# Optimization experiments

Hardware: AMD Instinct MI355X
Metric: run time of the kernel (lower is better)

Reference implementation:

```python
import jax, jax.numpy as jnp
import numpy as np

H = 16        # query heads
D = 4         # KV downsampling -> H//D = 4 kv heads
WINDOW = 1024 # sliding window
THETA = 10000.0


def _rope_cos_sin(L, dim):
    freqs = 1.0 / (THETA ** (jnp.arange(0, dim - 1, 2, dtype=jnp.float32) / dim))
    ang = jnp.arange(L, dtype=jnp.float32)[:, None] * freqs[None, :]  # (L, dim//2)
    return jnp.cos(ang), jnp.sin(ang)


def _apply_rope(x, cos, sin):
    # x: (N, h, L, dim); interleaved complex pairs (even=real, odd=imag)
    xr, xi = x[..., 0::2], x[..., 1::2]
    orr = xr * cos - xi * sin
    oii = xr * sin + xi * cos
    return jnp.stack([orr, oii], axis=-1).reshape(x.shape)


def setup_inputs() -> dict:
    key = jax.random.key(0)
    ks = jax.random.split(key, 5)
    N, L, E = 4, 2048, 2048
    return {
        "x": jax.random.normal(ks[0], (N, L, E), dtype=jnp.float32),
        "Wq": jax.random.normal(ks[1], (E, E), dtype=jnp.float32) * 0.02,
        "Wk": jax.random.normal(ks[2], (E // D, E), dtype=jnp.float32) * 0.02,
        "Wv": jax.random.normal(ks[3], (E // D, E), dtype=jnp.float32) * 0.02,
        "Wo": jax.random.normal(ks[4], (E, E), dtype=jnp.float32) * 0.02,
    }


def reference(x, Wq, Wk, Wv, Wo):
    N, L, E = x.shape
    dim = E // H  # 128 per-head dim (same for q and downsampled k/v)
    Hkv = H // D

    q = (x @ Wq.T).reshape(N, L, H, dim).transpose(0, 2, 1, 3)      # (N,H,L,d)
    k = (x @ Wk.T).reshape(N, L, Hkv, dim).transpose(0, 2, 1, 3)    # (N,Hkv,L,d)
    v = (x @ Wv.T).reshape(N, L, Hkv, dim).transpose(0, 2, 1, 3)

    cos, sin = _rope_cos_sin(L, dim)
    q = _apply_rope(q, cos, sin)
    k = _apply_rope(k, cos, sin)

    # GQA: expand kv heads (repeat_interleave along head axis)
    k = jnp.repeat(k, D, axis=1)  # (N,H,L,d)
    v = jnp.repeat(v, D, axis=1)

    scale = 1.0 / jnp.sqrt(jnp.float32(dim))
    attn = jnp.einsum("bhld,bhsd->bhls", q, k) * scale  # (N,H,L,L)

    i = jnp.arange(L)[:, None]
    j = jnp.arange(L)[None, :]
    allowed = (j <= i) & (j > i - WINDOW)  # causal + sliding window
    attn = jnp.where(allowed[None, None], attn, -jnp.inf)
    attn = jax.nn.softmax(attn, axis=-1)

    z = jnp.einsum("bhls,bhsd->bhld", attn, v)  # (N,H,L,d)
    z = z.transpose(0, 2, 1, 3).reshape(N, L, E)
    return z @ Wo.T
```

## Files before the change

kernel.cpp:

```cpp
#include <hip/hip_runtime.h>
#include <hip/hip_bf16.h>
#include <math.h>

typedef unsigned short u16;
typedef unsigned int u32;
typedef __attribute__((ext_vector_type(8))) short short8;
typedef __attribute__((ext_vector_type(8))) u16 ushort8;
typedef __attribute__((ext_vector_type(4))) float f32x4;
typedef __attribute__((ext_vector_type(16))) float f32x16;
typedef __attribute__((ext_vector_type(4))) u32 u32x4;

#define N_B 4
#define L_S 2048
#define E_D 2048
#define NH 16
#define HD 128
#define WIN 1024
#define QW 3072
#define LOG2E 1.4426950408889634f

static __device__ __forceinline__ u16 f32_bf16(float f) {
  u32 u = __builtin_bit_cast(u32, f);
  u = (u + 0x7fffu + ((u >> 16) & 1u)) >> 16;
  return (u16)u;
}
static __device__ __forceinline__ float bf16_f32(u16 h) {
  u32 u = ((u32)h) << 16;
  return __builtin_bit_cast(float, u);
}
static __device__ __forceinline__ u32 pack_bf16_pair(float lo, float hi) {
  __hip_bfloat162 h2 = __float22bfloat162_rn(make_float2(lo, hi));
  u32 r;
  __builtin_memcpy(&r, &h2, 4);
  return r;
}
static __device__ __forceinline__ void gload_lds16(const void* g, void* l) {
  __builtin_amdgcn_global_load_lds((__attribute__((address_space(1))) void*)g,
                                   (__attribute__((address_space(3))) void*)l, 16, 0, 0);
}

__global__ void k_cast(const float* __restrict__ src, u16* __restrict__ dst, int n8) {
  int i = blockIdx.x * blockDim.x + threadIdx.x;
  if (i >= n8) return;
  const float4* s = (const float4*)src + (size_t)i * 2;
  float4 a = s[0], b = s[1];
  ushort8 v;
  v[0] = f32_bf16(a.x); v[1] = f32_bf16(a.y); v[2] = f32_bf16(a.z); v[3] = f32_bf16(a.w);
  v[4] = f32_bf16(b.x); v[5] = f32_bf16(b.y); v[6] = f32_bf16(b.z); v[7] = f32_bf16(b.w);
  *((ushort8*)dst + i) = v;
}

__global__ void k_rope_table(float* __restrict__ cs, float* __restrict__ sn) {
  int idx = blockIdx.x * blockDim.x + threadIdx.x;
  int l = idx >> 6, f = idx & 63;
  float freq = exp2f(-(float)f * (13.287712379549449f / 64.0f));
  float ang = (float)l * freq;
  cs[idx] = cosf(ang);
  sn[idx] = sinf(ang);
}

__global__ void k_rope_apply(u16* __restrict__ QKV, const float* __restrict__ cs,
                             const float* __restrict__ sn) {
  int idx = blockIdx.x * blockDim.x + threadIdx.x;
  int f = idx & 63;
  int rest = idx >> 6;
  int hh = rest % 20;
  int row = rest / 20;
  int l = row & (L_S - 1);
  int col = (hh < NH) ? (hh * HD + 2 * f) : (E_D + (hh - NH) * HD + 2 * f);
  u32* p = (u32*)(QKV + (size_t)row * QW + col);
  u32 v = *p;
  float xr = bf16_f32((u16)(v & 0xffffu));
  float xi = bf16_f32((u16)(v >> 16));
  float c = cs[l * 64 + f], s = sn[l * 64 + f];
  float orr = xr * c - xi * s;
  float oii = xr * s + xi * c;
  *p = (u32)f32_bf16(orr) | ((u32)f32_bf16(oii) << 16);
}

template <int OUT_F32>
__global__ __launch_bounds__(512, 1) void k_gemm256(
    const u16* __restrict__ A, int lda,
    const u16* __restrict__ B, int ldb,
    void* __restrict__ Cp, int ldc, int K) {
  __shared__ __align__(16) u16 Ab[3 * 8192];
  __shared__ __align__(16) u16 Bb[3 * 8192];
  const int tid = threadIdx.x;
  const int lane = tid & 63, w = tid >> 6;
  const int lr = lane & 15, lg = lane >> 4;
  const int wm = w >> 2, wn = w & 3;
  const int fid = blockIdx.x;
  const int cc = fid & 7, l = fid >> 3;
  const int m0 = (cc * 4 + (l & 3)) * 256;
  const int n0 = (l >> 2) * 256;
  const int rswz = (lr & 6) << 3;

  auto STAGE = [&](int kt, int bb) {
    const int r2 = tid >> 2;
    const int ce = (((tid & 3) * 16) ^ ((r2 & 6) << 3)) >> 1;
#pragma unroll
    for (int rr = 0; rr < 2; ++rr) {
      int row = rr * 128 + r2;
      gload_lds16(A + (size_t)(m0 + row) * lda + kt * 32 + ce,
                  (char*)Ab + bb * 16384 + rr * 8192 + (w << 10));
      gload_lds16(B + (size_t)(n0 + row) * ldb + kt * 32 + ce,
                  (char*)Bb + bb * 16384 + rr * 8192 + (w << 10));
    }
  };

  f32x4 acc[8][4];
  const f32x4 z4 = {0.f, 0.f, 0.f, 0.f};
#pragma unroll
  for (int mf = 0; mf < 8; ++mf)
#pragma unroll
    for (int nf = 0; nf < 4; ++nf) acc[mf][nf] = z4;

  const int nt = K >> 5;
  STAGE(0, 0);
  STAGE(1, 1);
  asm volatile("s_waitcnt vmcnt(4)" ::: "memory");
  __builtin_amdgcn_sched_barrier(0);
  __builtin_amdgcn_s_barrier();
  __builtin_amdgcn_sched_barrier(0);

  int c3 = 0;
  for (int t = 0; t < nt; ++t) {
    int ib = c3 + 2; if (ib >= 3) ib -= 3;
    if (t + 2 < nt) STAGE(t + 2, ib);
    const char* Abt = (const char*)Ab + c3 * 16384;
    const char* Bbt = (const char*)Bb + c3 * 16384;
    short8 af[8], bf[4];
#pragma unroll
    for (int nf = 0; nf < 4; ++nf) {
      int row = wn * 64 + nf * 16 + lr;
      bf[nf] = *(const short8*)(Bbt + row * 64 + ((lg * 16) ^ rswz));
    }
#pragma unroll
    for (int mf = 0; mf < 8; ++mf) {
      int row = wm * 128 + mf * 16 + lr;
      af[mf] = *(const short8*)(Abt + row * 64 + ((lg * 16) ^ rswz));
    }
    __builtin_amdgcn_s_setprio(1);
#pragma unroll
    for (int mf = 0; mf < 8; ++mf)
#pragma unroll
      for (int nf = 0; nf < 4; ++nf)
        acc[mf][nf] =
            __builtin_amdgcn_mfma_f32_16x16x32_bf16(af[mf], bf[nf], acc[mf][nf], 0, 0, 0);
    __builtin_amdgcn_s_setprio(0);
    if (t + 2 < nt)
      asm volatile("s_waitcnt vmcnt(4) lgkmcnt(0)" ::: "memory");
    else
      asm volatile("s_waitcnt vmcnt(0) lgkmcnt(0)" ::: "memory");
    __builtin_amdgcn_sched_barrier(0);
    __builtin_amdgcn_s_barrier();
    __builtin_amdgcn_sched_barrier(0);
    c3 = (c3 == 2) ? 0 : c3 + 1;
  }

#pragma unroll
  for (int mf = 0; mf < 8; ++mf)
#pragma unroll
    for (int nf = 0; nf < 4; ++nf)
#pragma unroll
      for (int j = 0; j < 4; ++j) {
        size_t r = (size_t)(m0 + wm * 128 + mf * 16 + lg * 4 + j);
        int c = n0 + wn * 64 + nf * 16 + lr;
        if (OUT_F32)
          ((float*)Cp)[r * ldc + c] = acc[mf][nf][j];
        else
          ((u16*)Cp)[r * ldc + c] = f32_bf16(acc[mf][nf][j]);
      }
}

__global__ __launch_bounds__(512, 2) void k_attn(u16* __restrict__ QKV) {
  const int bx = blockIdx.x, h = blockIdx.y, b = blockIdx.z;
  const int qb = (b >= 2) ? 7 - bx : bx;
  const int tid = threadIdx.x;
  const int lane = tid & 63, w = tid >> 6;
  const int l31 = lane & 31, hi = lane >> 5;
  const int kh = h >> 2;
  const int qs = qb * 256 + w * 32;
  __shared__ __align__(16) u16 Klds[2][64 * 128];
  __shared__ __align__(16) u16 Vt[2][128 * 64];
  const float SCL2 = 0.08838834764831845f * 1.4426950408889634f;
  const size_t bL = (size_t)b * L_S;
  const int q = qs + l31;
  const size_t rowQ = (bL + q) * QW + h * HD;
  short8 qf[8];
#pragma unroll
  for (int ds = 0; ds < 8; ++ds)
    qf[ds] = *(const short8*)(QKV + rowQ + ds * 16 + hi * 8);
  f32x16 o[4];
#pragma unroll
  for (int dt = 0; dt < 4; ++dt)
#pragma unroll
    for (int r = 0; r < 16; ++r) o[dt][r] = 0.f;
  float m2 = -3e38f, lsum = 0.f;
  int t0 = qb * 256 - (WIN - 1);
  if (t0 < 0) t0 = 0;
  t0 >>= 6;
  const int t1 = 4 * qb + 3;
  short8 vreg[2];

  auto ISSUE_K = [&](int t, int buf) {
    char* Kb = (char*)Klds + buf * 16384;
#pragma unroll
    for (int rr = 0; rr < 2; ++rr) {
      int row = rr * 32 + (tid >> 4);
      int colb = ((tid & 15) * 16) ^ ((row & 7) << 4);
      gload_lds16(QKV + (bL + t * 64 + row) * QW + E_D + kh * HD + (colb >> 1),
                  Kb + rr * 8192 + w * 1024 + (lane << 4));
    }
  };
  auto LOAD_V = [&](int t) {
#pragma unroll
    for (int rr = 0; rr < 2; ++rr)
      vreg[rr] = *(const short8*)(QKV + (bL + t * 64 + lane) * QW + E_D + 512 + kh * HD +
                                  ((w * 2 + rr) * 8));
  };
  auto WRITE_V = [&](int buf) {
    char* Vb = (char*)Vt + buf * 16384;
#pragma unroll
    for (int rr = 0; rr < 2; ++rr) {
      int db = (w * 2 + rr) * 8;
#pragma unroll
      for (int e = 0; e < 8; ++e)
        *(u16*)(Vb + ((((db + e) * 128) + lane * 2) ^ (e << 4))) = (u16)vreg[rr][e];
    }
  };

  LOAD_V(t0);
  ISSUE_K(t0, 0);
  __syncthreads();
  WRITE_V(0);
  int c = 0;

  for (int t = t0; t <= t1; ++t) {
    const int kv0 = t * 64;
    const int tn = (t < t1) ? t + 1 : t1;
    ISSUE_K(tn, c ^ 1);
    LOAD_V(tn);
    const bool act = (kv0 <= qs + 31) && (kv0 + 63 > qs - WIN);
    u32x4 pa[4];
    if (act) {
      char* Kb = (char*)Klds + c * 16384;
      f32x16 s[2];
#pragma unroll
      for (int g = 0; g < 2; ++g)
#pragma unroll
        for (int r = 0; r < 16; ++r) s[g][r] = 0.f;
#pragma unroll
      for (int g = 0; g < 2; ++g) {
        const int r = g * 32 + l31;
        const int rsw = (r & 7) << 4;
#pragma unroll
        for (int ds = 0; ds < 8; ++ds) {
          short8 kf = *(const short8*)(Kb + (r * 256 + ((ds * 32 + hi * 16) ^ rsw)));
          s[g] = __builtin_amdgcn_mfma_f32_32x32x16_bf16(kf, qf[ds], s[g], 0, 0, 0);
        }
      }
      float v[2][16];
      float mx = -3e38f;
#pragma unroll
      for (int g = 0; g < 2; ++g)
#pragma unroll
        for (int r = 0; r < 16; ++r) {
          int kg = kv0 + g * 32 + (r & 3) + 8 * (r >> 2) + 4 * hi;
          bool a = (kg <= q) && (kg > q - WIN);
          float vv = a ? s[g][r] * SCL2 : -3e38f;
          v[g][r] = vv;
          mx = fmaxf(mx, vv);
        }
      mx = fmaxf(mx, __shfl_xor(mx, 32));
      if (__ballot(mx > m2 + 11.5415603f)) {
        float mn = fmaxf(m2, mx);
        float alpha = exp2f(m2 - mn);
        m2 = mn;
        lsum *= alpha;
#pragma unroll
        for (int r = 0; r < 16; ++r) {
          float alr = __shfl(alpha, (r & 3) + 8 * (r >> 2) + 4 * hi);
#pragma unroll
          for (int dt = 0; dt < 4; ++dt) o[dt][r] *= alr;
        }
      }
      float rs = 0.f;
#pragma unroll
      for (int g = 0; g < 2; ++g)
#pragma unroll
        for (int r = 0; r < 16; ++r) {
          float pe = (v[g][r] > -1e37f) ? exp2f(v[g][r] - m2) : 0.f;
          v[g][r] = pe;
          rs += pe;
        }
      rs += __shfl_xor(rs, 32);
      lsum += rs;
#pragma unroll
      for (int g = 0; g < 2; ++g) {
        u32 W[8];
#pragma unroll
        for (int qi = 0; qi < 4; ++qi) {
          W[2 * qi]     = pack_bf16_pair(v[g][4 * qi + 0], v[g][4 * qi + 1]);
          W[2 * qi + 1] = pack_bf16_pair(v[g][4 * qi + 2], v[g][4 * qi + 3]);
        }
        u32 R[4];
        R[0] = __shfl_xor(hi ? W[0] : W[2], 32);
        R[1] = __shfl_xor(hi ? W[1] : W[3], 32);
        R[2] = __shfl_xor(hi ? W[4] : W[6], 32);
        R[3] = __shfl_xor(hi ? W[5] : W[7], 32);
#pragma unroll
        for (int ksl = 0; ksl < 2; ++ksl) {
          u32x4 fr;
          if (hi == 0) {
            fr[0] = W[4 * ksl]; fr[1] = W[4 * ksl + 1];
            fr[2] = R[2 * ksl]; fr[3] = R[2 * ksl + 1];
          } else {
            fr[0] = R[2 * ksl]; fr[1] = R[2 * ksl + 1];
            fr[2] = W[4 * ksl + 2]; fr[3] = W[4 * ksl + 3];
          }
          pa[g * 2 + ksl] = fr;
        }
      }
    }
    __syncthreads();
    WRITE_V(c ^ 1);
    if (act) {
      char* Vb = (char*)Vt + c * 16384;
      __builtin_amdgcn_s_setprio(1);
#pragma unroll
      for (int dt = 0; dt < 4; ++dt) {
        const int d = dt * 32 + l31;
        const int dsw = (d & 7) << 4;
#pragma unroll
        for (int ks = 0; ks < 4; ++ks) {
          short8 vf = *(const short8*)(Vb + (d * 128 + ((ks * 32 + hi * 16) ^ dsw)));
          o[dt] = __builtin_amdgcn_mfma_f32_32x32x16_bf16(
              __builtin_bit_cast(short8, pa[ks]), vf, o[dt], 0, 0, 0);
        }
      }
      __builtin_amdgcn_s_setprio(0);
    }
    c ^= 1;
  }
  float inv = 1.0f / lsum;
#pragma unroll
  for (int r = 0; r < 16; ++r) {
    int ridx = (r & 3) + 8 * (r >> 2) + 4 * hi;
    float invr = __shfl(inv, ridx);
    size_t rowO = (bL + qs + ridx) * QW + h * HD + l31;
#pragma unroll
    for (int dt = 0; dt < 4; ++dt)
      QKV[rowO + dt * 32] = f32_bf16(o[dt][r] * invr);
  }
}

extern "C" void kernel_launch(void* const* d_in, const int* in_sizes, int n_in,
                              void* d_out, int out_size, void* d_ws, size_t ws_size,
                              hipStream_t stream) {
  const float* x  = (const float*)d_in[0];
  const float* Wq = (const float*)d_in[1];
  const float* Wk = (const float*)d_in[2];
  const float* Wv = (const float*)d_in[3];
  const float* Wo = (const float*)d_in[4];
  char* ws = (char*)d_ws;
  if (ws_size < 105906176u) return;
  u16* xb    = (u16*)(ws);
  u16* Wqkv  = (u16*)(ws + 33554432);
  u16* Wob   = (u16*)(ws + 46137344);
  u16* QKV   = (u16*)(ws + 54525952);
  float* cs  = (float*)(ws + 104857600);
  float* sn  = (float*)(ws + 105381888);

  k_cast<<<8192, 256, 0, stream>>>(x, xb, 16777216 / 8);
  k_cast<<<2048, 256, 0, stream>>>(Wq, Wqkv, 4194304 / 8);
  k_cast<<<512, 256, 0, stream>>>(Wk, Wqkv + 2048 * 2048, 1048576 / 8);
  k_cast<<<512, 256, 0, stream>>>(Wv, Wqkv + 2560 * 2048, 1048576 / 8);
  k_cast<<<2048, 256, 0, stream>>>(Wo, Wob, 4194304 / 8);
  k_rope_table<<<512, 256, 0, stream>>>(cs, sn);
  k_gemm256<0><<<384, 512, 0, stream>>>(xb, 2048, Wqkv, 2048, QKV, QW, 2048);
  k_rope_apply<<<40960, 256, 0, stream>>>(QKV, cs, sn);
  k_attn<<<dim3(8, 16, 4), 512, 0, stream>>>(QKV);
  k_gemm256<1><<<256, 512, 0, stream>>>(QKV, QW, Wob, 2048, d_out, 2048, 2048);
}
```

Before: 427.3 us.

## Fuse Q RoPE into attention, split GEMM k-step, skip masking on full tiles

Query RoPE now runs inside the attention kernel as the Q fragments are loaded, so the standalone RoPE pass only touches the K heads, which saves a read-modify-write over Q. The GEMM main loop is split into two half-M phases with extra barriers, interleaving the A and B global-to-LDS staging with the MFMA work. The attention kernel adds a fast path for fully unmasked tiles that skips per-element mask checks, and it no longer issues a redundant prefetch or V write on the last iteration. The extra barriers in the GEMM could add synchronisation stalls.

```diff
diff --git a/kernel.cpp b/kernel.cpp
--- a/kernel.cpp
+++ b/kernel.cpp
@@ -59,15 +59,15 @@
   sn[idx] = sinf(ang);
 }
 
-__global__ void k_rope_apply(u16* __restrict__ QKV, const float* __restrict__ cs,
-                             const float* __restrict__ sn) {
+__global__ void k_rope_k(u16* __restrict__ QKV, const float* __restrict__ cs,
+                         const float* __restrict__ sn) {
   int idx = blockIdx.x * blockDim.x + threadIdx.x;
   int f = idx & 63;
   int rest = idx >> 6;
-  int hh = rest % 20;
-  int row = rest / 20;
+  int hh = rest & 3;
+  int row = rest >> 2;
   int l = row & (L_S - 1);
-  int col = (hh < NH) ? (hh * HD + 2 * f) : (E_D + (hh - NH) * HD + 2 * f);
+  int col = E_D + hh * HD + 2 * f;
   u32* p = (u32*)(QKV + (size_t)row * QW + col);
   u32 v = *p;
   float xr = bf16_f32((u16)(v & 0xffffu));
@@ -79,7 +79,7 @@
 }
 
 template <int OUT_F32>
-__global__ __launch_bounds__(512, 1) void k_gemm256(
+__global__ __launch_bounds__(512, 1) void k_gemm8(
     const u16* __restrict__ A, int lda,
     const u16* __restrict__ B, int ldb,
     void* __restrict__ Cp, int ldc, int K) {
@@ -95,17 +95,19 @@
   const int n0 = (l >> 2) * 256;
   const int rswz = (lr & 6) << 3;
 
-  auto STAGE = [&](int kt, int bb) {
-    const int r2 = tid >> 2;
-    const int ce = (((tid & 3) * 16) ^ ((r2 & 6) << 3)) >> 1;
-#pragma unroll
-    for (int rr = 0; rr < 2; ++rr) {
-      int row = rr * 128 + r2;
-      gload_lds16(A + (size_t)(m0 + row) * lda + kt * 32 + ce,
+  const int r2 = tid >> 2;
+  const int ce = (((tid & 3) * 16) ^ ((r2 & 6) << 3)) >> 1;
+  auto STAGE_A = [&](int kt, int bb) {
+#pragma unroll
+    for (int rr = 0; rr < 2; ++rr)
+      gload_lds16(A + (size_t)(m0 + rr * 128 + r2) * lda + kt * 32 + ce,
                   (char*)Ab + bb * 16384 + rr * 8192 + (w << 10));
-      gload_lds16(B + (size_t)(n0 + row) * ldb + kt * 32 + ce,
+  };
+  auto STAGE_B = [&](int kt, int bb) {
+#pragma unroll
+    for (int rr = 0; rr < 2; ++rr)
+      gload_lds16(B + (size_t)(n0 + rr * 128 + r2) * ldb + kt * 32 + ce,
                   (char*)Bb + bb * 16384 + rr * 8192 + (w << 10));
-    }
   };
 
   f32x4 acc[8][4];
@@ -116,8 +118,8 @@
     for (int nf = 0; nf < 4; ++nf) acc[mf][nf] = z4;
 
   const int nt = K >> 5;
-  STAGE(0, 0);
-  STAGE(1, 1);
+  STAGE_A(0, 0); STAGE_B(0, 0);
+  STAGE_A(1, 1); STAGE_B(1, 1);
   asm volatile("s_waitcnt vmcnt(4)" ::: "memory");
   __builtin_amdgcn_sched_barrier(0);
   __builtin_amdgcn_s_barrier();
@@ -126,32 +128,57 @@
   int c3 = 0;
   for (int t = 0; t < nt; ++t) {
     int ib = c3 + 2; if (ib >= 3) ib -= 3;
-    if (t + 2 < nt) STAGE(t + 2, ib);
     const char* Abt = (const char*)Ab + c3 * 16384;
     const char* Bbt = (const char*)Bb + c3 * 16384;
-    short8 af[8], bf[4];
+    short8 af[4], bf[4];
 #pragma unroll
     for (int nf = 0; nf < 4; ++nf) {
       int row = wn * 64 + nf * 16 + lr;
       bf[nf] = *(const short8*)(Bbt + row * 64 + ((lg * 16) ^ rswz));
     }
 #pragma unroll
-    for (int mf = 0; mf < 8; ++mf) {
+    for (int mf = 0; mf < 4; ++mf) {
       int row = wm * 128 + mf * 16 + lr;
       af[mf] = *(const short8*)(Abt + row * 64 + ((lg * 16) ^ rswz));
     }
+    if (t + 2 < nt) STAGE_A(t + 2, ib);
+    __builtin_amdgcn_sched_barrier(0);
+    __builtin_amdgcn_s_barrier();
+    asm volatile("s_waitcnt lgkmcnt(0)" ::: "memory");
+    __builtin_amdgcn_sched_barrier(0);
     __builtin_amdgcn_s_setprio(1);
 #pragma unroll
-    for (int mf = 0; mf < 8; ++mf)
+    for (int mf = 0; mf < 4; ++mf)
 #pragma unroll
       for (int nf = 0; nf < 4; ++nf)
         acc[mf][nf] =
             __builtin_amdgcn_mfma_f32_16x16x32_bf16(af[mf], bf[nf], acc[mf][nf], 0, 0, 0);
     __builtin_amdgcn_s_setprio(0);
+    __builtin_amdgcn_sched_barrier(0);
+    __builtin_amdgcn_s_barrier();
+    __builtin_amdgcn_sched_barrier(0);
+#pragma unroll
+    for (int mf = 0; mf < 4; ++mf) {
+      int row = wm * 128 + 64 + mf * 16 + lr;
+      af[mf] = *(const short8*)(Abt + row * 64 + ((lg * 16) ^ rswz));
+    }
+    if (t + 2 < nt) STAGE_B(t + 2, ib);
     if (t + 2 < nt)
-      asm volatile("s_waitcnt vmcnt(4) lgkmcnt(0)" ::: "memory");
+      asm volatile("s_waitcnt vmcnt(4)" ::: "memory");
     else
-      asm volatile("s_waitcnt vmcnt(0) lgkmcnt(0)" ::: "memory");
+      asm volatile("s_waitcnt vmcnt(0)" ::: "memory");
+    __builtin_amdgcn_sched_barrier(0);
+    __builtin_amdgcn_s_barrier();
+    asm volatile("s_waitcnt lgkmcnt(0)" ::: "memory");
+    __builtin_amdgcn_sched_barrier(0);
+    __builtin_amdgcn_s_setprio(1);
+#pragma unroll
+    for (int mf = 0; mf < 4; ++mf)
+#pragma unroll
+      for (int nf = 0; nf < 4; ++nf)
+        acc[4 + mf][nf] =
+            __builtin_amdgcn_mfma_f32_16x16x32_bf16(af[mf], bf[nf], acc[4 + mf][nf], 0, 0, 0);
+    __builtin_amdgcn_s_setprio(0);
     __builtin_amdgcn_sched_barrier(0);
     __builtin_amdgcn_s_barrier();
     __builtin_amdgcn_sched_barrier(0);
@@ -173,7 +200,9 @@
       }
 }
 
-__global__ __launch_bounds__(512, 2) void k_attn(u16* __restrict__ QKV) {
+__global__ __launch_bounds__(512, 2) void k_attn(u16* __restrict__ QKV,
+                                                 const float* __restrict__ cs,
+                                                 const float* __restrict__ sn) {
   const int bx = blockIdx.x, h = blockIdx.y, b = blockIdx.z;
   const int qb = (b >= 2) ? 7 - bx : bx;
   const int tid = threadIdx.x;
@@ -189,8 +218,23 @@
   const size_t rowQ = (bL + q) * QW + h * HD;
   short8 qf[8];
 #pragma unroll
-  for (int ds = 0; ds < 8; ++ds)
-    qf[ds] = *(const short8*)(QKV + rowQ + ds * 16 + hi * 8);
+  for (int ds = 0; ds < 8; ++ds) {
+    short8 qr = *(const short8*)(QKV + rowQ + ds * 16 + hi * 8);
+    const int f0 = ds * 8 + hi * 4;
+    float4 c4 = *(const float4*)(cs + (size_t)q * 64 + f0);
+    float4 s4 = *(const float4*)(sn + (size_t)q * 64 + f0);
+    ushort8 qo;
+#pragma unroll
+    for (int e = 0; e < 4; ++e) {
+      float xr = bf16_f32((u16)qr[2 * e]);
+      float xi = bf16_f32((u16)qr[2 * e + 1]);
+      float co = (e == 0) ? c4.x : (e == 1) ? c4.y : (e == 2) ? c4.z : c4.w;
+      float si = (e == 0) ? s4.x : (e == 1) ? s4.y : (e == 2) ? s4.z : s4.w;
+      qo[2 * e]     = f32_bf16(xr * co - xi * si);
+      qo[2 * e + 1] = f32_bf16(xr * si + xi * co);
+    }
+    qf[ds] = __builtin_bit_cast(short8, qo);
+  }
   f32x16 o[4];
 #pragma unroll
   for (int dt = 0; dt < 4; ++dt)
@@ -238,10 +282,13 @@
 
   for (int t = t0; t <= t1; ++t) {
     const int kv0 = t * 64;
-    const int tn = (t < t1) ? t + 1 : t1;
-    ISSUE_K(tn, c ^ 1);
-    LOAD_V(tn);
+    const bool lastt = (t == t1);
+    if (!lastt) {
+      ISSUE_K(t + 1, c ^ 1);
+      LOAD_V(t + 1);
+    }
     const bool act = (kv0 <= qs + 31) && (kv0 + 63 > qs - WIN);
+    const bool full = (kv0 + 63 <= qs) && (kv0 > qs + 31 - WIN);
     u32x4 pa[4];
     if (act) {
       char* Kb = (char*)Klds + c * 16384;
@@ -262,16 +309,27 @@
       }
       float v[2][16];
       float mx = -3e38f;
-#pragma unroll
-      for (int g = 0; g < 2; ++g)
-#pragma unroll
-        for (int r = 0; r < 16; ++r) {
-          int kg = kv0 + g * 32 + (r & 3) + 8 * (r >> 2) + 4 * hi;
-          bool a = (kg <= q) && (kg > q - WIN);
-          float vv = a ? s[g][r] * SCL2 : -3e38f;
-          v[g][r] = vv;
-          mx = fmaxf(mx, vv);
-        }
+      if (full) {
+#pragma unroll
+        for (int g = 0; g < 2; ++g)
+#pragma unroll
+          for (int r = 0; r < 16; ++r) {
+            float vv = s[g][r] * SCL2;
+            v[g][r] = vv;
+            mx = fmaxf(mx, vv);
+          }
+      } else {
+#pragma unroll
+        for (int g = 0; g < 2; ++g)
+#pragma unroll
+          for (int r = 0; r < 16; ++r) {
+            int kg = kv0 + g * 32 + (r & 3) + 8 * (r >> 2) + 4 * hi;
+            bool a = (kg <= q) && (kg > q - WIN);
+            float vv = a ? s[g][r] * SCL2 : -3e38f;
+            v[g][r] = vv;
+            mx = fmaxf(mx, vv);
+          }
+      }
       mx = fmaxf(mx, __shfl_xor(mx, 32));
       if (__ballot(mx > m2 + 11.5415603f)) {
         float mn = fmaxf(m2, mx);
@@ -286,14 +344,25 @@
         }
       }
       float rs = 0.f;
-#pragma unroll
-      for (int g = 0; g < 2; ++g)
-#pragma unroll
-        for (int r = 0; r < 16; ++r) {
-          float pe = (v[g][r] > -1e37f) ? exp2f(v[g][r] - m2) : 0.f;
-          v[g][r] = pe;
-          rs += pe;
-        }
+      if (full) {
+#pragma unroll
+        for (int g = 0; g < 2; ++g)
+#pragma unroll
+          for (int r = 0; r < 16; ++r) {
+            float pe = exp2f(v[g][r] - m2);
+            v[g][r] = pe;
+            rs += pe;
+          }
+      } else {
+#pragma unroll
+        for (int g = 0; g < 2; ++g)
+#pragma unroll
+          for (int r = 0; r < 16; ++r) {
+            float pe = (v[g][r] > -1e37f) ? exp2f(v[g][r] - m2) : 0.f;
+            v[g][r] = pe;
+            rs += pe;
+          }
+      }
       rs += __shfl_xor(rs, 32);
       lsum += rs;
 #pragma unroll
@@ -324,7 +393,6 @@
       }
     }
     __syncthreads();
-    WRITE_V(c ^ 1);
     if (act) {
       char* Vb = (char*)Vt + c * 16384;
       __builtin_amdgcn_s_setprio(1);
@@ -341,6 +409,7 @@
       }
       __builtin_amdgcn_s_setprio(0);
     }
+    if (!lastt) WRITE_V(c ^ 1);
     c ^= 1;
   }
   float inv = 1.0f / lsum;
@@ -378,8 +447,8 @@
   k_cast<<<512, 256, 0, stream>>>(Wv, Wqkv + 2560 * 2048, 1048576 / 8);
   k_cast<<<2048, 256, 0, stream>>>(Wo, Wob, 4194304 / 8);
   k_rope_table<<<512, 256, 0, stream>>>(cs, sn);
-  k_gemm256<0><<<384, 512, 0, stream>>>(xb, 2048, Wqkv, 2048, QKV, QW, 2048);
-  k_rope_apply<<<40960, 256, 0, stream>>>(QKV, cs, sn);
-  k_attn<<<dim3(8, 16, 4), 512, 0, stream>>>(QKV);
-  k_gemm256<1><<<256, 512, 0, stream>>>(QKV, QW, Wob, 2048, d_out, 2048, 2048);
-}
+  k_gemm8<0><<<384, 512, 0, stream>>>(xb, 2048, Wqkv, 2048, QKV, QW, 2048);
+  k_rope_k<<<8192, 256, 0, stream>>>(QKV, cs, sn);
+  k_attn<<<dim3(8, 16, 4), 512, 0, stream>>>(QKV, cs, sn);
+  k_gemm8<1><<<256, 512, 0, stream>>>(QKV, QW, Wob, 2048, d_out, 2048, 2048);
+}
```

Result: faster. 376.0 us (-12.0%).
